# Kernel tuning notes

Hardware: AMD Instinct MI355X
Metric: run time of the kernel (lower is better)

The kernel has to match this reference:

```python
import jax, jax.numpy as jnp
import numpy as np

B, S, R, E, H = 2, 2048, 128, 2048, 16
D = E // H  # head_dim = 128


def _ste(x, q):
    # straight-through estimator: forward=q, backward=identity
    return x + jax.lax.stop_gradient(q - x)


def quant_weight(w):
    # BitNet b1.58-style ternary weight quantization with mean-abs scale
    scale = jnp.clip(jnp.mean(jnp.abs(w)), 1e-5, None)
    q = jnp.clip(jnp.round(w / scale), -1.0, 1.0) * scale
    return _ste(w, q)


def quant_act(x):
    # per-token 8-bit absmax activation quantization
    s = 127.0 / jnp.clip(jnp.max(jnp.abs(x), axis=-1, keepdims=True), 1e-5, None)
    q = jnp.clip(jnp.round(x * s), -128.0, 127.0) / s
    return _ste(x, q)


def quantized_linear(x, w):
    # dequantized low-bit matmul: Xq @ Wq^T
    return quant_act(x) @ quant_weight(w).T


def setup_inputs() -> dict:
    key = jax.random.key(0)
    ks = jax.random.split(key, 8)
    sc = 1.0 / np.sqrt(E)
    return {
        "x": jax.random.normal(ks[0], (B, S, E), dtype=jnp.float32),
        "reasoning_tokens": jax.random.normal(ks[1], (B, R, E), dtype=jnp.float32),
        "q_w": jax.random.normal(ks[2], (E, E), dtype=jnp.float32) * sc,
        "k_w": jax.random.normal(ks[3], (E, E), dtype=jnp.float32) * sc,
        "v_w": jax.random.normal(ks[4], (E, E), dtype=jnp.float32) * sc,
        "out_w": jax.random.normal(ks[5], (E, E), dtype=jnp.float32) * sc,
        "out_b": jnp.zeros((E,), dtype=jnp.float32),
    }


def _heads(t):
    b, s, _ = t.shape
    return t.reshape(b, s, H, D).transpose(0, 2, 1, 3)  # [B,H,S,D]


def reference(x, reasoning_tokens, q_w, k_w, v_w, out_w, out_b):
    b, s, e = x.shape
    # quantized QKV projections (dequant + matmul)
    q = _heads(quantized_linear(x, q_w))
    k = _heads(quantized_linear(x, k_w))
    v = _heads(quantized_linear(x, v_w))
    # reasoning tokens go through the UNquantized projections (per source)
    rk = _heads(reasoning_tokens @ k_w.T)
    rv = _heads(reasoning_tokens @ v_w.T)
    k = jnp.concatenate([k, rk], axis=2)  # [B,H,S+R,D]
    v = jnp.concatenate([v, rv], axis=2)
    scores = jnp.einsum('bhqd,bhkd->bhqk', q, k) / np.sqrt(D).astype(np.float32)
    attn = jax.nn.softmax(scores, axis=-1)
    o = jnp.einsum('bhqk,bhkd->bhqd', attn, v)
    o = o.transpose(0, 2, 1, 3).reshape(b, s, e)
    return o @ out_w.T + out_b
```

## Files before the change

kernel.cpp:

```cpp
#include <hip/hip_runtime.h>


typedef __bf16 bf16;
typedef __bf16 bf16x8 __attribute__((ext_vector_type(8)));
typedef float  f32x4  __attribute__((ext_vector_type(4)));
typedef int    i32x4  __attribute__((ext_vector_type(4)));
typedef char   char8  __attribute__((ext_vector_type(8)));

#define B_   2
#define S_   2048
#define R_   128
#define E_   2048
#define H_   16
#define D_   128
#define NKV  2176
#define NTOK 4096
#define KDIM 2048

typedef const __attribute__((address_space(1))) void* gas_ptr;
typedef __attribute__((address_space(3))) void*       las_ptr;

__device__ __forceinline__ void load_lds16(const void* g, void* l) {
  __builtin_amdgcn_global_load_lds((gas_ptr)g, (las_ptr)l, 16, 0, 0);
}

__global__ __launch_bounds__(256) void abs_sum_k(
    const float* __restrict__ w0, const float* __restrict__ w1,
    const float* __restrict__ w2, double* wsD) {
  int z = blockIdx.y;
  const float* w = z == 0 ? w0 : (z == 1 ? w1 : w2);
  int tid = threadIdx.x;
  size_t base = ((size_t)blockIdx.x * 256 + tid) * 8;
  f32x4 a = *(const f32x4*)(w + base);
  f32x4 b = *(const f32x4*)(w + base + 4);
  float s = 0.f;
#pragma unroll
  for (int j = 0; j < 4; j++) s += fabsf(a[j]) + fabsf(b[j]);
  double d = (double)s;
#pragma unroll
  for (int m = 1; m < 64; m <<= 1) d += __shfl_xor(d, m);
  __shared__ double red[4];
  if ((tid & 63) == 0) red[tid >> 6] = d;
  __syncthreads();
  if (tid == 0) atomicAdd(&wsD[z], red[0] + red[1] + red[2] + red[3]);
}

__global__ __launch_bounds__(256) void prep_k(
    const float* __restrict__ qw, const float* __restrict__ kw,
    const float* __restrict__ vw, const float* __restrict__ ow,
    const float* __restrict__ rt, const double* __restrict__ wsD, float* wsF,
    char* __restrict__ TQ8, char* __restrict__ TK8, char* __restrict__ TV8,
    bf16* __restrict__ KWb, bf16* __restrict__ VWb, bf16* __restrict__ OWb,
    bf16* __restrict__ RTb) {
  int y = blockIdx.y;
  if (y < 3) {
    const float* w = y == 0 ? qw : (y == 1 ? kw : vw);
    char* t        = y == 0 ? TQ8 : (y == 1 ? TK8 : TV8);
    float scale = (float)fmax(wsD[y] * (1.0 / 4194304.0), 1e-5);
    if (blockIdx.x == 0 && threadIdx.x == 0) wsF[y] = scale;
    size_t base = ((size_t)blockIdx.x * 256 + threadIdx.x) * 8;
    f32x4 a = *(const f32x4*)(w + base);
    f32x4 b = *(const f32x4*)(w + base + 4);
    float rs = 1.0f / scale;
    char8 o;
#pragma unroll
    for (int j = 0; j < 8; j++) {
      float v = j < 4 ? a[j] : b[j - 4];
      float q = rintf(v * rs);
      q = fminf(fmaxf(q, -1.f), 1.f);
      o[j] = (char)(int)q;
    }
    *(char8*)(t + base) = o;
  } else {
    if (y == 6 && blockIdx.x >= 256) return;
    const float* src = y == 3 ? kw : (y == 4 ? vw : (y == 5 ? ow : rt));
    bf16* dst        = y == 3 ? KWb : (y == 4 ? VWb : (y == 5 ? OWb : RTb));
    size_t i = ((size_t)blockIdx.x * 256 + threadIdx.x) * 8;
    f32x4 a = *(const f32x4*)(src + i);
    f32x4 b = *(const f32x4*)(src + i + 4);
    bf16x8 o;
#pragma unroll
    for (int j = 0; j < 4; j++) { o[j] = (bf16)a[j]; o[j + 4] = (bf16)b[j]; }
    *(bf16x8*)(dst + i) = o;
  }
}

__global__ __launch_bounds__(256) void actq_k(
    const float* __restrict__ x, char* __restrict__ xq,
    float* __restrict__ aScale) {
  int row = blockIdx.x, tid = threadIdx.x;
  const float* xr = x + (size_t)row * E_;
  f32x4 a = *(const f32x4*)(xr + tid * 8);
  f32x4 b = *(const f32x4*)(xr + tid * 8 + 4);
  float am = 0.f;
#pragma unroll
  for (int j = 0; j < 4; j++) am = fmaxf(am, fmaxf(fabsf(a[j]), fabsf(b[j])));
#pragma unroll
  for (int m = 1; m < 64; m <<= 1) am = fmaxf(am, __shfl_xor(am, m));
  __shared__ float red[4];
  if ((tid & 63) == 0) red[tid >> 6] = am;
  __syncthreads();
  float mx = fmaxf(fmaxf(red[0], red[1]), fmaxf(red[2], red[3]));
  float maxC = fmaxf(mx, 1e-5f);
  float s = 127.0f / maxC;
  char8 o;
#pragma unroll
  for (int j = 0; j < 8; j++) {
    float v = j < 4 ? a[j] : b[j - 4];
    float q = rintf(v * s);
    q = fminf(fmaxf(q, -128.f), 127.f);
    o[j] = (char)(int)q;
  }
  *(char8*)(xq + (size_t)row * E_ + tid * 8) = o;
  if (tid == 0) aScale[row] = maxC / 127.0f;
}

__device__ __forceinline__ void gemm_core(const bf16* Arow, const bf16* Brow,
                                          bf16* As, bf16* Bs, int tid,
                                          f32x4 acc[4][4]) {
  int wave = tid >> 6, lane = tid & 63, quad = lane >> 4, l16 = lane & 15;
  int wm = wave >> 1, wn = wave & 1;
  const char* aT = (const char*)Arow;
  const char* bT = (const char*)Brow;
  int c1 = tid + 256;
  size_t aO0 = (size_t)(tid >> 2) * (KDIM * 2) + (size_t)(tid & 3) * 16;
  size_t aO1 = (size_t)(c1 >> 2) * (KDIM * 2) + (size_t)(c1 & 3) * 16;
  char* AsB = (char*)As;
  char* BsB = (char*)Bs;
  int wofs = wave * 1024;
  for (int k0 = 0; k0 < KDIM; k0 += 32) {
    __syncthreads();
    load_lds16(aT + aO0, AsB + wofs);
    load_lds16(aT + aO1, AsB + 4096 + wofs);
    load_lds16(bT + aO0, BsB + wofs);
    load_lds16(bT + aO1, BsB + 4096 + wofs);
    aT += 64;
    bT += 64;
    __syncthreads();
    bf16x8 af[4], bfr[4];
#pragma unroll
    for (int mt = 0; mt < 4; mt++)
      af[mt] = *(const bf16x8*)(As + (wm * 64 + mt * 16 + l16) * 32 + quad * 8);
#pragma unroll
    for (int nt = 0; nt < 4; nt++)
      bfr[nt] = *(const bf16x8*)(Bs + (wn * 64 + nt * 16 + l16) * 32 + quad * 8);
#pragma unroll
    for (int mt = 0; mt < 4; mt++)
#pragma unroll
      for (int nt = 0; nt < 4; nt++)
        acc[mt][nt] = __builtin_amdgcn_mfma_f32_16x16x32_bf16(
            af[mt], bfr[nt], acc[mt][nt], 0, 0, 0);
  }
}

__device__ __forceinline__ void gemm_core_i8(const char* Arow, const char* Brow,
                                             char* As, char* Bs, int tid,
                                             i32x4 acc[4][4]) {
  int wave = tid >> 6, lane = tid & 63, quad = lane >> 4, l16 = lane & 15;
  int wm = wave >> 1, wn = wave & 1;
  int s0 = tid, s1 = tid + 256;
  int r0 = s0 >> 2, r1 = s1 >> 2;
  size_t aO0 = (size_t)r0 * KDIM + (size_t)((s0 & 3) ^ (r0 & 3)) * 16;
  size_t aO1 = (size_t)r1 * KDIM + (size_t)((s1 & 3) ^ (r1 & 3)) * 16;
  const char* aT = Arow;
  const char* bT = Brow;
  int wofs = wave * 1024;
  int cs = (quad ^ (l16 & 3)) * 16;
  for (int k0 = 0; k0 < KDIM; k0 += 64) {
    __syncthreads();
    load_lds16(aT + aO0, As + wofs);
    load_lds16(aT + aO1, As + 4096 + wofs);
    load_lds16(bT + aO0, Bs + wofs);
    load_lds16(bT + aO1, Bs + 4096 + wofs);
    aT += 64;
    bT += 64;
    __syncthreads();
    i32x4 af[4], bfr[4];
#pragma unroll
    for (int mt = 0; mt < 4; mt++)
      af[mt] = *(const i32x4*)(As + (wm * 64 + mt * 16 + l16) * 64 + cs);
#pragma unroll
    for (int nt = 0; nt < 4; nt++)
      bfr[nt] = *(const i32x4*)(Bs + (wn * 64 + nt * 16 + l16) * 64 + cs);
#pragma unroll
    for (int mt = 0; mt < 4; mt++)
#pragma unroll
      for (int nt = 0; nt < 4; nt++)
        acc[mt][nt] = __builtin_amdgcn_mfma_i32_16x16x64_i8(
            af[mt], bfr[nt], acc[mt][nt], 0, 0, 0);
  }
}

__global__ __launch_bounds__(256) void gemm_qk(
    const char* __restrict__ XQ8, const char* __restrict__ TQ8,
    const char* __restrict__ TK8, const bf16* __restrict__ RTb,
    const bf16* __restrict__ KWb, const float* __restrict__ asc,
    const float* __restrict__ wsF, bf16* __restrict__ QB,
    bf16* __restrict__ KB) {
  __shared__ char As[8192];
  __shared__ char Bs[8192];
  int m0 = blockIdx.x * 128, n0 = blockIdx.y * 128;
  bool isQ = n0 < 2048;
  bool isRsn = m0 >= NTOK;
  if (isQ && isRsn) return;
  int tid = threadIdx.x;
  int lane = tid & 63, quad = lane >> 4, l16 = lane & 15;
  int wm = (tid >> 6) >> 1, wn = (tid >> 6) & 1;

  if (!isRsn) {
    const char* Bm = isQ ? (TQ8 + (size_t)n0 * KDIM)
                         : (TK8 + (size_t)(n0 - 2048) * KDIM);
    float sW = isQ ? wsF[0] : wsF[1];
    i32x4 acc[4][4];
    const i32x4 iz = {0, 0, 0, 0};
#pragma unroll
    for (int i = 0; i < 4; i++)
#pragma unroll
      for (int j = 0; j < 4; j++) acc[i][j] = iz;
    gemm_core_i8(XQ8 + (size_t)m0 * KDIM, Bm, As, Bs, tid, acc);
#pragma unroll
    for (int mt = 0; mt < 4; mt++) {
      int mB = m0 + wm * 64 + mt * 16 + quad * 4;
#pragma unroll
      for (int nt = 0; nt < 4; nt++) {
        int n = n0 + wn * 64 + nt * 16 + l16;
        int nn = n & 2047, h = nn >> 7, d = nn & 127;
#pragma unroll
        for (int r = 0; r < 4; r++) {
          int m = mB + r;
          float v = (float)acc[mt][nt][r] * asc[m] * sW;
          int tb = m >> 11, ts = m & 2047;
          if (isQ)
            QB[((size_t)((tb * 16 + h) * S_ + ts)) * 128 + d] = (bf16)v;
          else
            KB[((size_t)((tb * 16 + h) * NKV + ts)) * 128 + d] = (bf16)v;
        }
      }
    }
  } else {
    f32x4 acc[4][4];
    const f32x4 fz = {0.f, 0.f, 0.f, 0.f};
#pragma unroll
    for (int i = 0; i < 4; i++)
#pragma unroll
      for (int j = 0; j < 4; j++) acc[i][j] = fz;
    gemm_core(RTb + (size_t)(m0 - NTOK) * KDIM,
              KWb + (size_t)(n0 - 2048) * KDIM, (bf16*)As, (bf16*)Bs, tid, acc);
#pragma unroll
    for (int mt = 0; mt < 4; mt++) {
      int mB = m0 + wm * 64 + mt * 16 + quad * 4;
#pragma unroll
      for (int nt = 0; nt < 4; nt++) {
        int n = n0 + wn * 64 + nt * 16 + l16;
        int nn = n & 2047, h = nn >> 7, d = nn & 127;
#pragma unroll
        for (int r = 0; r < 4; r++) {
          int j = mB + r - NTOK;
          int tb = j >> 7, ts = 2048 + (j & 127);
          KB[((size_t)((tb * 16 + h) * NKV + ts)) * 128 + d] =
              (bf16)acc[mt][nt][r];
        }
      }
    }
  }
}

__global__ __launch_bounds__(256) void gemm_vt(
    const char* __restrict__ TV8, const char* __restrict__ XQ8,
    const bf16* __restrict__ VWb, const bf16* __restrict__ RTb,
    const float* __restrict__ asc, const float* __restrict__ wsF,
    bf16* __restrict__ VT) {
  __shared__ char As[8192];
  __shared__ char Bs[8192];
  int m0 = blockIdx.x * 128, n0 = blockIdx.y * 128;
  bool isRsn = n0 >= NTOK;
  int tid = threadIdx.x;
  int lane = tid & 63, quad = lane >> 4, l16 = lane & 15;
  int wm = (tid >> 6) >> 1, wn = (tid >> 6) & 1;

  if (!isRsn) {
    i32x4 acc[4][4];
    const i32x4 iz = {0, 0, 0, 0};
#pragma unroll
    for (int i = 0; i < 4; i++)
#pragma unroll
      for (int j = 0; j < 4; j++) acc[i][j] = iz;
    gemm_core_i8(TV8 + (size_t)m0 * KDIM, XQ8 + (size_t)n0 * KDIM, As, Bs,
                 tid, acc);
#pragma unroll
    for (int mt = 0; mt < 4; mt++) {
      int mB = m0 + wm * 64 + mt * 16 + quad * 4;
#pragma unroll
      for (int nt = 0; nt < 4; nt++) {
        int n = n0 + wn * 64 + nt * 16 + l16;
        float sb = asc[n] * wsF[2];
        int tb = n >> 11, ts = n & 2047;
#pragma unroll
        for (int r = 0; r < 4; r++) {
          int m = mB + r, h = m >> 7, d = m & 127;
          VT[((size_t)((tb * 16 + h) * 128 + d)) * NKV + ts] =
              (bf16)((float)acc[mt][nt][r] * sb);
        }
      }
    }
  } else {
    f32x4 acc[4][4];
    const f32x4 fz = {0.f, 0.f, 0.f, 0.f};
#pragma unroll
    for (int i = 0; i < 4; i++)
#pragma unroll
      for (int j = 0; j < 4; j++) acc[i][j] = fz;
    gemm_core(VWb + (size_t)m0 * KDIM, RTb + (size_t)(n0 - NTOK) * KDIM,
              (bf16*)As, (bf16*)Bs, tid, acc);
#pragma unroll
    for (int mt = 0; mt < 4; mt++) {
      int mB = m0 + wm * 64 + mt * 16 + quad * 4;
#pragma unroll
      for (int nt = 0; nt < 4; nt++) {
        int n = n0 + wn * 64 + nt * 16 + l16;
        int j = n - NTOK, tb = j >> 7, ts = 2048 + (j & 127);
#pragma unroll
        for (int r = 0; r < 4; r++) {
          int m = mB + r, h = m >> 7, d = m & 127;
          VT[((size_t)((tb * 16 + h) * 128 + d)) * NKV + ts] =
              (bf16)acc[mt][nt][r];
        }
      }
    }
  }
}

__global__ __launch_bounds__(256) void gemm_out(
    const bf16* __restrict__ A, const bf16* __restrict__ Bm,
    const float* __restrict__ bias, float* __restrict__ out) {
  __shared__ bf16 As[128 * 32];
  __shared__ bf16 Bs[128 * 32];
  int m0 = blockIdx.x * 128, n0 = blockIdx.y * 128;
  int tid = threadIdx.x;
  int lane = tid & 63, quad = lane >> 4, l16 = lane & 15;
  int wm = (tid >> 6) >> 1, wn = (tid >> 6) & 1;

  f32x4 acc[4][4];
  const f32x4 fz = {0.f, 0.f, 0.f, 0.f};
#pragma unroll
  for (int i = 0; i < 4; i++)
#pragma unroll
    for (int j = 0; j < 4; j++) acc[i][j] = fz;
  gemm_core(A + (size_t)m0 * KDIM, Bm + (size_t)n0 * KDIM, As, Bs, tid, acc);

#pragma unroll
  for (int mt = 0; mt < 4; mt++) {
    int mB = m0 + wm * 64 + mt * 16 + quad * 4;
#pragma unroll
    for (int nt = 0; nt < 4; nt++) {
      int n = n0 + wn * 64 + nt * 16 + l16;
      float bv = bias[n];
#pragma unroll
      for (int r = 0; r < 4; r++)
        out[(size_t)(mB + r) * E_ + n] = acc[mt][nt][r] + bv;
    }
  }
}

__global__ __launch_bounds__(256) void attn_k(
    const bf16* __restrict__ q, const bf16* __restrict__ k,
    const bf16* __restrict__ vt, bf16* __restrict__ o) {
  __shared__ bf16 Ks[64 * 128];
  __shared__ bf16 Vs[128 * 64];
  __shared__ bf16 Ps[128 * 64];
  const float SC = 0.08838834764831845f;
  const float SHIFT = 12.0f;
  int tid = threadIdx.x;
  int wave = tid >> 6, lane = tid & 63, quad = lane >> 4, l16 = lane & 15;
  int bh = blockIdx.y, q0 = blockIdx.x * 128;

  const bf16* qb = q + ((size_t)bh * S_ + q0) * D_;
  const char* kb = (const char*)(k + (size_t)bh * NKV * D_);
  const char* vb = (const char*)(vt + (size_t)bh * D_ * NKV);

  bf16x8 qf[2][4];
#pragma unroll
  for (int qt = 0; qt < 2; qt++)
#pragma unroll
    for (int ds = 0; ds < 4; ds++)
      qf[qt][ds] = *(const bf16x8*)(qb +
                   (size_t)(wave * 32 + qt * 16 + l16) * D_ + ds * 32 + quad * 8);

  const f32x4 fz = {0.f, 0.f, 0.f, 0.f};
  f32x4 oa[2][8];
#pragma unroll
  for (int i = 0; i < 2; i++)
#pragma unroll
    for (int j = 0; j < 8; j++) oa[i][j] = fz;
  float lsum[2][4];
#pragma unroll
  for (int i = 0; i < 2; i++)
#pragma unroll
    for (int r = 0; r < 4; r++) lsum[i][r] = 0.f;

  char* KsB = (char*)Ks;
  char* VsB = (char*)Vs;
  char* PsB = (char*)Ps;

  int kRow[4], kC[4], vRow[4], vC[4];
#pragma unroll
  for (int i = 0; i < 4; i++) {
    int slot = i * 256 + tid;
    kRow[i] = slot >> 4;
    kC[i] = (slot & 15) ^ (kRow[i] & 15);
    vRow[i] = slot >> 3;
    vC[i] = (slot & 7) ^ (vRow[i] & 7);
  }
  int wofs = wave * 1024;

  for (int kv = 0; kv < NKV; kv += 64) {
    __syncthreads();
#pragma unroll
    for (int i = 0; i < 4; i++)
      load_lds16(kb + (size_t)(kv + kRow[i]) * 256 + kC[i] * 16,
                 KsB + i * 4096 + wofs);
#pragma unroll
    for (int i = 0; i < 4; i++)
      load_lds16(vb + (size_t)vRow[i] * (NKV * 2) + (size_t)kv * 2 + vC[i] * 16,
                 VsB + i * 4096 + wofs);
    __syncthreads();

    f32x4 s[2][4];
#pragma unroll
    for (int i = 0; i < 2; i++)
#pragma unroll
      for (int j = 0; j < 4; j++) s[i][j] = fz;
#pragma unroll
    for (int ds = 0; ds < 4; ds++) {
      bf16x8 kf[4];
#pragma unroll
      for (int kt = 0; kt < 4; kt++) {
        int row = kt * 16 + l16;
        int c = (ds * 4 + quad) ^ (row & 15);
        kf[kt] = *(const bf16x8*)(KsB + row * 256 + c * 16);
      }
#pragma unroll
      for (int qt = 0; qt < 2; qt++)
#pragma unroll
        for (int kt = 0; kt < 4; kt++)
          s[qt][kt] = __builtin_amdgcn_mfma_f32_16x16x32_bf16(
              qf[qt][ds], kf[kt], s[qt][kt], 0, 0, 0);
    }

#pragma unroll
    for (int qt = 0; qt < 2; qt++)
#pragma unroll
      for (int kt = 0; kt < 4; kt++)
#pragma unroll
        for (int r = 0; r < 4; r++)
          s[qt][kt][r] = __expf(s[qt][kt][r] * SC - SHIFT);
#pragma unroll
    for (int qt = 0; qt < 2; qt++)
#pragma unroll
      for (int r = 0; r < 4; r++)
        lsum[qt][r] += (s[qt][0][r] + s[qt][1][r]) + (s[qt][2][r] + s[qt][3][r]);

#pragma unroll
    for (int qt = 0; qt < 2; qt++)
#pragma unroll
      for (int kt = 0; kt < 4; kt++)
#pragma unroll
        for (int r = 0; r < 4; r++) {
          int row = wave * 32 + qt * 16 + quad * 4 + r;
          int col = kt * 16 + l16;
          int c = (col >> 3) ^ (row & 7);
          *(bf16*)(PsB + row * 128 + c * 16 + (col & 7) * 2) =
              (bf16)s[qt][kt][r];
        }
    __syncthreads();

#pragma unroll
    for (int ks = 0; ks < 2; ks++) {
      bf16x8 pf[2], vf[8];
#pragma unroll
      for (int qt = 0; qt < 2; qt++) {
        int row = wave * 32 + qt * 16 + l16;
        int c = (ks * 4 + quad) ^ (row & 7);
        pf[qt] = *(const bf16x8*)(PsB + row * 128 + c * 16);
      }
#pragma unroll
      for (int dt = 0; dt < 8; dt++) {
        int row = dt * 16 + l16;
        int c = (ks * 4 + quad) ^ (row & 7);
        vf[dt] = *(const bf16x8*)(VsB + row * 128 + c * 16);
      }
#pragma unroll
      for (int qt = 0; qt < 2; qt++)
#pragma unroll
        for (int dt = 0; dt < 8; dt++)
          oa[qt][dt] = __builtin_amdgcn_mfma_f32_16x16x32_bf16(
              pf[qt], vf[dt], oa[qt][dt], 0, 0, 0);
    }
  }

  int b = bh >> 4, h = bh & 15;
#pragma unroll
  for (int qt = 0; qt < 2; qt++) {
    float rl[4];
#pragma unroll
    for (int r = 0; r < 4; r++) {
      float l = lsum[qt][r];
#pragma unroll
      for (int msk = 1; msk < 16; msk <<= 1) l += __shfl_xor(l, msk);
      rl[r] = 1.0f / l;
    }
#pragma unroll
    for (int dt = 0; dt < 8; dt++)
#pragma unroll
      for (int r = 0; r < 4; r++) {
        int srow = q0 + wave * 32 + qt * 16 + quad * 4 + r;
        int col = h * 128 + dt * 16 + l16;
        o[((size_t)(b * S_ + srow)) * E_ + col] = (bf16)(oa[qt][dt][r] * rl[r]);
      }
  }
}

static constexpr size_t O_ASC = 256;
static constexpr size_t O_XQ8 = 32768;
static constexpr size_t O_RTB = O_XQ8 + 8388608;
static constexpr size_t O_TQ8 = O_RTB + 1048576;
static constexpr size_t O_TK8 = O_TQ8 + 4194304;
static constexpr size_t O_TV8 = O_TK8 + 4194304;
static constexpr size_t O_KWB = O_TV8 + 4194304;
static constexpr size_t O_VWB = O_KWB + 8388608;
static constexpr size_t O_OWB = O_VWB + 8388608;
static constexpr size_t O_QB  = O_OWB + 8388608;
static constexpr size_t O_KB  = O_QB + 16777216;
static constexpr size_t O_VT  = O_KB + 17825792;
static constexpr size_t O_OB  = O_XQ8;
static constexpr size_t WS_NEED = O_VT + 17825792;

extern "C" void kernel_launch(void* const* d_in, const int* in_sizes, int n_in,
                              void* d_out, int out_size, void* d_ws,
                              size_t ws_size, hipStream_t stream) {
  const float* x  = (const float*)d_in[0];
  const float* rt = (const float*)d_in[1];
  const float* qw = (const float*)d_in[2];
  const float* kw = (const float*)d_in[3];
  const float* vw = (const float*)d_in[4];
  const float* ow = (const float*)d_in[5];
  const float* ob = (const float*)d_in[6];
  char* ws = (char*)d_ws;
  if (ws_size < WS_NEED) return;

  double* wsD = (double*)ws;
  float* wsF  = (float*)(ws + 64);
  float* asc  = (float*)(ws + O_ASC);
  char* XQ8 = ws + O_XQ8;
  bf16* RTb = (bf16*)(ws + O_RTB);
  char* TQ8 = ws + O_TQ8;
  char* TK8 = ws + O_TK8;
  char* TV8 = ws + O_TV8;
  bf16* KWb = (bf16*)(ws + O_KWB);
  bf16* VWb = (bf16*)(ws + O_VWB);
  bf16* OWb = (bf16*)(ws + O_OWB);
  bf16* QB  = (bf16*)(ws + O_QB);
  bf16* KB  = (bf16*)(ws + O_KB);
  bf16* VT  = (bf16*)(ws + O_VT);
  bf16* OB  = (bf16*)(ws + O_OB);
  float* out = (float*)d_out;

  hipMemsetAsync(ws, 0, 64, stream);
  abs_sum_k<<<dim3(2048, 3), 256, 0, stream>>>(qw, kw, vw, wsD);
  prep_k<<<dim3(2048, 7), 256, 0, stream>>>(qw, kw, vw, ow, rt, wsD, wsF,
                                            TQ8, TK8, TV8, KWb, VWb, OWb, RTb);
  actq_k<<<4096, 256, 0, stream>>>(x, XQ8, asc);

  gemm_qk<<<dim3(34, 32), 256, 0, stream>>>(XQ8, TQ8, TK8, RTb, KWb, asc, wsF,
                                            QB, KB);
  gemm_vt<<<dim3(16, 34), 256, 0, stream>>>(TV8, XQ8, VWb, RTb, asc, wsF, VT);

  attn_k<<<dim3(16, 32), 256, 0, stream>>>(QB, KB, VT, OB);

  gemm_out<<<dim3(32, 16), 256, 0, stream>>>(OB, OWb, ob, out);
}
```

Measured before the change: 558.2 us.

## Split attention KV range across two blocks and merge QK/V projection launches

Attention now runs with a third grid dimension that splits the 2176 keys into two halves. Each half writes an unnormalized partial output plus its row sum. A new combine kernel adds the two partials and normalizes them into the head-interleaved layout. The intent is to double the number of attention blocks so more compute units stay busy. Separately, the Q/K and V^T projection GEMMs are fused into one launch, removing a kernel boundary and letting both sets of tiles share the device. The cost is an extra pass over the partial outputs and extra workspace. The merge is only correct if both halves use a common softmax max reference.

```diff
diff --git a/kernel.cpp b/kernel.cpp
--- a/kernel.cpp
+++ b/kernel.cpp
@@ -14,6 +14,7 @@
 #define H_   16
 #define D_   128
 #define NKV  2176
+#define HKV  1088
 #define NTOK 4096
 #define KDIM 2048
 
@@ -191,139 +192,131 @@
   }
 }
 
-__global__ __launch_bounds__(256) void gemm_qk(
+__global__ __launch_bounds__(256) void gemm_proj(
     const char* __restrict__ XQ8, const char* __restrict__ TQ8,
-    const char* __restrict__ TK8, const bf16* __restrict__ RTb,
-    const bf16* __restrict__ KWb, const float* __restrict__ asc,
+    const char* __restrict__ TK8, const char* __restrict__ TV8,
+    const bf16* __restrict__ RTb, const bf16* __restrict__ KWb,
+    const bf16* __restrict__ VWb, const float* __restrict__ asc,
     const float* __restrict__ wsF, bf16* __restrict__ QB,
-    bf16* __restrict__ KB) {
+    bf16* __restrict__ KB, bf16* __restrict__ VT) {
   __shared__ char As[8192];
   __shared__ char Bs[8192];
-  int m0 = blockIdx.x * 128, n0 = blockIdx.y * 128;
-  bool isQ = n0 < 2048;
-  bool isRsn = m0 >= NTOK;
-  if (isQ && isRsn) return;
   int tid = threadIdx.x;
   int lane = tid & 63, quad = lane >> 4, l16 = lane & 15;
   int wm = (tid >> 6) >> 1, wn = (tid >> 6) & 1;
 
-  if (!isRsn) {
-    const char* Bm = isQ ? (TQ8 + (size_t)n0 * KDIM)
-                         : (TK8 + (size_t)(n0 - 2048) * KDIM);
-    float sW = isQ ? wsF[0] : wsF[1];
-    i32x4 acc[4][4];
-    const i32x4 iz = {0, 0, 0, 0};
-#pragma unroll
-    for (int i = 0; i < 4; i++)
-#pragma unroll
-      for (int j = 0; j < 4; j++) acc[i][j] = iz;
-    gemm_core_i8(XQ8 + (size_t)m0 * KDIM, Bm, As, Bs, tid, acc);
-#pragma unroll
-    for (int mt = 0; mt < 4; mt++) {
-      int mB = m0 + wm * 64 + mt * 16 + quad * 4;
-#pragma unroll
-      for (int nt = 0; nt < 4; nt++) {
-        int n = n0 + wn * 64 + nt * 16 + l16;
-        int nn = n & 2047, h = nn >> 7, d = nn & 127;
-#pragma unroll
-        for (int r = 0; r < 4; r++) {
-          int m = mB + r;
-          float v = (float)acc[mt][nt][r] * asc[m] * sW;
-          int tb = m >> 11, ts = m & 2047;
-          if (isQ)
-            QB[((size_t)((tb * 16 + h) * S_ + ts)) * 128 + d] = (bf16)v;
-          else
-            KB[((size_t)((tb * 16 + h) * NKV + ts)) * 128 + d] = (bf16)v;
+  if (blockIdx.y < 32) {
+    int m0 = blockIdx.x * 128, n0 = blockIdx.y * 128;
+    bool isQ = n0 < 2048;
+    bool isRsn = m0 >= NTOK;
+    if (isQ && isRsn) return;
+    if (!isRsn) {
+      const char* Bm = isQ ? (TQ8 + (size_t)n0 * KDIM)
+                           : (TK8 + (size_t)(n0 - 2048) * KDIM);
+      float sW = isQ ? wsF[0] : wsF[1];
+      i32x4 acc[4][4];
+      const i32x4 iz = {0, 0, 0, 0};
+#pragma unroll
+      for (int i = 0; i < 4; i++)
+#pragma unroll
+        for (int j = 0; j < 4; j++) acc[i][j] = iz;
+      gemm_core_i8(XQ8 + (size_t)m0 * KDIM, Bm, As, Bs, tid, acc);
+#pragma unroll
+      for (int mt = 0; mt < 4; mt++) {
+        int mB = m0 + wm * 64 + mt * 16 + quad * 4;
+#pragma unroll
+        for (int nt = 0; nt < 4; nt++) {
+          int n = n0 + wn * 64 + nt * 16 + l16;
+          int nn = n & 2047, h = nn >> 7, d = nn & 127;
+#pragma unroll
+          for (int r = 0; r < 4; r++) {
+            int m = mB + r;
+            float v = (float)acc[mt][nt][r] * asc[m] * sW;
+            int tb = m >> 11, ts = m & 2047;
+            if (isQ)
+              QB[((size_t)((tb * 16 + h) * S_ + ts)) * 128 + d] = (bf16)v;
+            else
+              KB[((size_t)((tb * 16 + h) * NKV + ts)) * 128 + d] = (bf16)v;
+          }
         }
       }
+    } else {
+      f32x4 acc[4][4];
+      const f32x4 fz = {0.f, 0.f, 0.f, 0.f};
+#pragma unroll
+      for (int i = 0; i < 4; i++)
+#pragma unroll
+        for (int j = 0; j < 4; j++) acc[i][j] = fz;
+      gemm_core(RTb + (size_t)(m0 - NTOK) * KDIM,
+                KWb + (size_t)(n0 - 2048) * KDIM, (bf16*)As, (bf16*)Bs, tid,
+                acc);
+#pragma unroll
+      for (int mt = 0; mt < 4; mt++) {
+        int mB = m0 + wm * 64 + mt * 16 + quad * 4;
+#pragma unroll
+        for (int nt = 0; nt < 4; nt++) {
+          int n = n0 + wn * 64 + nt * 16 + l16;
+          int nn = n & 2047, h = nn >> 7, d = nn & 127;
+#pragma unroll
+          for (int r = 0; r < 4; r++) {
+            int j = mB + r - NTOK;
+            int tb = j >> 7, ts = 2048 + (j & 127);
+            KB[((size_t)((tb * 16 + h) * NKV + ts)) * 128 + d] =
+                (bf16)acc[mt][nt][r];
+          }
+        }
+      }
     }
   } else {
-    f32x4 acc[4][4];
-    const f32x4 fz = {0.f, 0.f, 0.f, 0.f};
-#pragma unroll
-    for (int i = 0; i < 4; i++)
-#pragma unroll
-      for (int j = 0; j < 4; j++) acc[i][j] = fz;
-    gemm_core(RTb + (size_t)(m0 - NTOK) * KDIM,
-              KWb + (size_t)(n0 - 2048) * KDIM, (bf16*)As, (bf16*)Bs, tid, acc);
-#pragma unroll
-    for (int mt = 0; mt < 4; mt++) {
-      int mB = m0 + wm * 64 + mt * 16 + quad * 4;
-#pragma unroll
-      for (int nt = 0; nt < 4; nt++) {
-        int n = n0 + wn * 64 + nt * 16 + l16;
-        int nn = n & 2047, h = nn >> 7, d = nn & 127;
-#pragma unroll
-        for (int r = 0; r < 4; r++) {
-          int j = mB + r - NTOK;
-          int tb = j >> 7, ts = 2048 + (j & 127);
-          KB[((size_t)((tb * 16 + h) * NKV + ts)) * 128 + d] =
-              (bf16)acc[mt][nt][r];
+    int m0 = (blockIdx.y - 32) * 128, n0 = blockIdx.x * 128;
+    bool isRsn = n0 >= NTOK;
+    if (!isRsn) {
+      i32x4 acc[4][4];
+      const i32x4 iz = {0, 0, 0, 0};
+#pragma unroll
+      for (int i = 0; i < 4; i++)
+#pragma unroll
+        for (int j = 0; j < 4; j++) acc[i][j] = iz;
+      gemm_core_i8(TV8 + (size_t)m0 * KDIM, XQ8 + (size_t)n0 * KDIM, As, Bs,
+                   tid, acc);
+#pragma unroll
+      for (int mt = 0; mt < 4; mt++) {
+        int mB = m0 + wm * 64 + mt * 16 + quad * 4;
+#pragma unroll
+        for (int nt = 0; nt < 4; nt++) {
+          int n = n0 + wn * 64 + nt * 16 + l16;
+          float sb = asc[n] * wsF[2];
+          int tb = n >> 11, ts = n & 2047;
+#pragma unroll
+          for (int r = 0; r < 4; r++) {
+            int m = mB + r, h = m >> 7, d = m & 127;
+            VT[((size_t)((tb * 16 + h) * 128 + d)) * NKV + ts] =
+                (bf16)((float)acc[mt][nt][r] * sb);
+          }
         }
       }
-    }
-  }
-}
-
-__global__ __launch_bounds__(256) void gemm_vt(
-    const char* __restrict__ TV8, const char* __restrict__ XQ8,
-    const bf16* __restrict__ VWb, const bf16* __restrict__ RTb,
-    const float* __restrict__ asc, const float* __restrict__ wsF,
-    bf16* __restrict__ VT) {
-  __shared__ char As[8192];
-  __shared__ char Bs[8192];
-  int m0 = blockIdx.x * 128, n0 = blockIdx.y * 128;
-  bool isRsn = n0 >= NTOK;
-  int tid = threadIdx.x;
-  int lane = tid & 63, quad = lane >> 4, l16 = lane & 15;
-  int wm = (tid >> 6) >> 1, wn = (tid >> 6) & 1;
-
-  if (!isRsn) {
-    i32x4 acc[4][4];
-    const i32x4 iz = {0, 0, 0, 0};
-#pragma unroll
-    for (int i = 0; i < 4; i++)
-#pragma unroll
-      for (int j = 0; j < 4; j++) acc[i][j] = iz;
-    gemm_core_i8(TV8 + (size_t)m0 * KDIM, XQ8 + (size_t)n0 * KDIM, As, Bs,
-                 tid, acc);
-#pragma unroll
-    for (int mt = 0; mt < 4; mt++) {
-      int mB = m0 + wm * 64 + mt * 16 + quad * 4;
-#pragma unroll
-      for (int nt = 0; nt < 4; nt++) {
-        int n = n0 + wn * 64 + nt * 16 + l16;
-        float sb = asc[n] * wsF[2];
-        int tb = n >> 11, ts = n & 2047;
-#pragma unroll
-        for (int r = 0; r < 4; r++) {
-          int m = mB + r, h = m >> 7, d = m & 127;
-          VT[((size_t)((tb * 16 + h) * 128 + d)) * NKV + ts] =
-              (bf16)((float)acc[mt][nt][r] * sb);
-        }
-      }
-    }
-  } else {
-    f32x4 acc[4][4];
-    const f32x4 fz = {0.f, 0.f, 0.f, 0.f};
-#pragma unroll
-    for (int i = 0; i < 4; i++)
-#pragma unroll
-      for (int j = 0; j < 4; j++) acc[i][j] = fz;
-    gemm_core(VWb + (size_t)m0 * KDIM, RTb + (size_t)(n0 - NTOK) * KDIM,
-              (bf16*)As, (bf16*)Bs, tid, acc);
-#pragma unroll
-    for (int mt = 0; mt < 4; mt++) {
-      int mB = m0 + wm * 64 + mt * 16 + quad * 4;
-#pragma unroll
-      for (int nt = 0; nt < 4; nt++) {
-        int n = n0 + wn * 64 + nt * 16 + l16;
-        int j = n - NTOK, tb = j >> 7, ts = 2048 + (j & 127);
-#pragma unroll
-        for (int r = 0; r < 4; r++) {
-          int m = mB + r, h = m >> 7, d = m & 127;
-          VT[((size_t)((tb * 16 + h) * 128 + d)) * NKV + ts] =
-              (bf16)acc[mt][nt][r];
+    } else {
+      f32x4 acc[4][4];
+      const f32x4 fz = {0.f, 0.f, 0.f, 0.f};
+#pragma unroll
+      for (int i = 0; i < 4; i++)
+#pragma unroll
+        for (int j = 0; j < 4; j++) acc[i][j] = fz;
+      gemm_core(VWb + (size_t)m0 * KDIM, RTb + (size_t)(n0 - NTOK) * KDIM,
+                (bf16*)As, (bf16*)Bs, tid, acc);
+#pragma unroll
+      for (int mt = 0; mt < 4; mt++) {
+        int mB = m0 + wm * 64 + mt * 16 + quad * 4;
+#pragma unroll
+        for (int nt = 0; nt < 4; nt++) {
+          int n = n0 + wn * 64 + nt * 16 + l16;
+          int j = n - NTOK, tb = j >> 7, ts = 2048 + (j & 127);
+#pragma unroll
+          for (int r = 0; r < 4; r++) {
+            int m = mB + r, h = m >> 7, d = m & 127;
+            VT[((size_t)((tb * 16 + h) * 128 + d)) * NKV + ts] =
+                (bf16)acc[mt][nt][r];
+          }
         }
       }
     }
@@ -364,7 +357,8 @@
 
 __global__ __launch_bounds__(256) void attn_k(
     const bf16* __restrict__ q, const bf16* __restrict__ k,
-    const bf16* __restrict__ vt, bf16* __restrict__ o) {
+    const bf16* __restrict__ vt, bf16* __restrict__ Op,
+    float* __restrict__ lp) {
   __shared__ bf16 Ks[64 * 128];
   __shared__ bf16 Vs[128 * 64];
   __shared__ bf16 Ps[128 * 64];
@@ -373,6 +367,7 @@
   int tid = threadIdx.x;
   int wave = tid >> 6, lane = tid & 63, quad = lane >> 4, l16 = lane & 15;
   int bh = blockIdx.y, q0 = blockIdx.x * 128;
+  int kv0 = blockIdx.z * HKV;
 
   const bf16* qb = q + ((size_t)bh * S_ + q0) * D_;
   const char* kb = (const char*)(k + (size_t)bh * NKV * D_);
@@ -413,7 +408,7 @@
   }
   int wofs = wave * 1024;
 
-  for (int kv = 0; kv < NKV; kv += 64) {
+  for (int kv = kv0; kv < kv0 + HKV; kv += 64) {
     __syncthreads();
 #pragma unroll
     for (int i = 0; i < 4; i++)
@@ -498,26 +493,45 @@
     }
   }
 
-  int b = bh >> 4, h = bh & 15;
+  size_t zofs = (size_t)blockIdx.z * ((size_t)B_ * H_ * S_);
 #pragma unroll
   for (int qt = 0; qt < 2; qt++) {
-    float rl[4];
 #pragma unroll
     for (int r = 0; r < 4; r++) {
       float l = lsum[qt][r];
 #pragma unroll
       for (int msk = 1; msk < 16; msk <<= 1) l += __shfl_xor(l, msk);
-      rl[r] = 1.0f / l;
+      if (l16 == 0) {
+        int srow = q0 + wave * 32 + qt * 16 + quad * 4 + r;
+        lp[zofs + (size_t)bh * S_ + srow] = l;
+      }
     }
 #pragma unroll
     for (int dt = 0; dt < 8; dt++)
 #pragma unroll
       for (int r = 0; r < 4; r++) {
         int srow = q0 + wave * 32 + qt * 16 + quad * 4 + r;
-        int col = h * 128 + dt * 16 + l16;
-        o[((size_t)(b * S_ + srow)) * E_ + col] = (bf16)(oa[qt][dt][r] * rl[r]);
-      }
-  }
+        int col = dt * 16 + l16;
+        Op[(zofs + (size_t)bh * S_ + srow) * 128 + col] = (bf16)oa[qt][dt][r];
+      }
+  }
+}
+
+__global__ __launch_bounds__(256) void combine_k(
+    const bf16* __restrict__ Op, const float* __restrict__ lp,
+    bf16* __restrict__ OB) {
+  int m = blockIdx.x, t = threadIdx.x;
+  int b = m >> 11, s = m & 2047;
+  int idx = t * 8, h = idx >> 7, d = idx & 127;
+  size_t rofs = ((size_t)(b * 16 + h) * S_ + s);
+  const size_t Z = (size_t)B_ * H_ * S_;
+  float rl = 1.0f / (lp[rofs] + lp[Z + rofs]);
+  bf16x8 o0 = *(const bf16x8*)(Op + rofs * 128 + d);
+  bf16x8 o1 = *(const bf16x8*)(Op + (Z + rofs) * 128 + d);
+  bf16x8 o;
+#pragma unroll
+  for (int j = 0; j < 8; j++) o[j] = (bf16)(((float)o0[j] + (float)o1[j]) * rl);
+  *(bf16x8*)(OB + (size_t)m * E_ + idx) = o;
 }
 
 static constexpr size_t O_ASC = 256;
@@ -532,8 +546,10 @@
 static constexpr size_t O_QB  = O_OWB + 8388608;
 static constexpr size_t O_KB  = O_QB + 16777216;
 static constexpr size_t O_VT  = O_KB + 17825792;
-static constexpr size_t O_OB  = O_XQ8;
 static constexpr size_t WS_NEED = O_VT + 17825792;
+static constexpr size_t O_OP = O_XQ8;
+static constexpr size_t O_LP = O_XQ8 + 33554432;
+static constexpr size_t O_OB = O_QB;
 
 extern "C" void kernel_launch(void* const* d_in, const int* in_sizes, int n_in,
                               void* d_out, int out_size, void* d_ws,
@@ -562,6 +578,8 @@
   bf16* QB  = (bf16*)(ws + O_QB);
   bf16* KB  = (bf16*)(ws + O_KB);
   bf16* VT  = (bf16*)(ws + O_VT);
+  bf16* Op  = (bf16*)(ws + O_OP);
+  float* lp = (float*)(ws + O_LP);
   bf16* OB  = (bf16*)(ws + O_OB);
   float* out = (float*)d_out;
 
@@ -571,11 +589,11 @@
                                             TQ8, TK8, TV8, KWb, VWb, OWb, RTb);
   actq_k<<<4096, 256, 0, stream>>>(x, XQ8, asc);
 
-  gemm_qk<<<dim3(34, 32), 256, 0, stream>>>(XQ8, TQ8, TK8, RTb, KWb, asc, wsF,
-                                            QB, KB);
-  gemm_vt<<<dim3(16, 34), 256, 0, stream>>>(TV8, XQ8, VWb, RTb, asc, wsF, VT);
-
-  attn_k<<<dim3(16, 32), 256, 0, stream>>>(QB, KB, VT, OB);
+  gemm_proj<<<dim3(34, 48), 256, 0, stream>>>(XQ8, TQ8, TK8, TV8, RTb, KWb,
+                                              VWb, asc, wsF, QB, KB, VT);
+
+  attn_k<<<dim3(16, 32, 2), 256, 0, stream>>>(QB, KB, VT, Op, lp);
+  combine_k<<<4096, 256, 0, stream>>>(Op, lp, OB);
 
   gemm_out<<<dim3(32, 16), 256, 0, stream>>>(OB, OWb, ob, out);
 }
```

After: 536.0 us. 4.0% less time.
